# Kernel tuning notes

Hardware: AMD Instinct MI355X
Metric: run time of the kernel (lower is better)

Reference implementation:

```python
import jax, jax.numpy as jnp
import numpy as np

PATCH = 8
EPS_LN = 1e-5
EPS_NORM = 1e-12


def conv1x1(x, w):
    # x: [b,i,h,w], w: [o,i]
    return jnp.einsum('bihw,oi->bohw', x, w)


def dwconv3(x, w):
    # depthwise 3x3, SAME padding; w: [C,1,3,3]
    return jax.lax.conv_general_dilated(
        x, w, window_strides=(1, 1), padding='SAME',
        feature_group_count=x.shape[1],
        dimension_numbers=('NCHW', 'OIHW', 'NCHW'))


def l2norm(x, axis=-1):
    n = jnp.sqrt(jnp.sum(x * x, axis=axis, keepdims=True))
    return x / jnp.maximum(n, EPS_NORM)


def layernorm_ch(x, w, b):
    # WithBias LayerNorm over the channel dim of NCHW (matches to_3d/to_4d)
    mu = jnp.mean(x, axis=1, keepdims=True)
    var = jnp.mean((x - mu) ** 2, axis=1, keepdims=True)
    return (x - mu) / jnp.sqrt(var + EPS_LN) * w[None, :, None, None] + b[None, :, None, None]


def patchify(t, p):
    b, c, h, w = t.shape
    t = t.reshape(b, c, h // p, p, w // p, p)
    return t.transpose(0, 1, 2, 4, 3, 5)  # b c gh gw p p


def unpatchify(t):
    b, c, gh, gw, p1, p2 = t.shape
    return t.transpose(0, 1, 2, 4, 3, 5).reshape(b, c, gh * p1, gw * p2)


def setup_inputs() -> dict:
    key = jax.random.key(0)
    ks = jax.random.split(key, 12)
    b, c, h, w = 4, 128, 256, 256
    heads = 8
    s = 0.05
    inp = {
        'x': jax.random.normal(ks[0], (b, c, h, w), jnp.float32),
        'qkv_w': s * jax.random.normal(ks[1], (3 * c, c), jnp.float32),
        'qkv_dw': s * jax.random.normal(ks[2], (3 * c, 1, 3, 3), jnp.float32),
        'proj_w': s * jax.random.normal(ks[3], (c, c), jnp.float32),
        'q1_w': s * jax.random.normal(ks[4], (c, c), jnp.float32),
        'q2_w': s * jax.random.normal(ks[5], (c, c), jnp.float32),
        'kv_w': s * jax.random.normal(ks[6], (2 * c, c), jnp.float32),
        'kv_dw': s * jax.random.normal(ks[7], (2 * c, 1, 3, 3), jnp.float32),
        'projf_w': s * jax.random.normal(ks[8], (c, c), jnp.float32),
        'temperature': jnp.ones((1, heads, 1, 1), jnp.float32),
        'ln_w': jnp.ones((c,), jnp.float32),
        'ln_b': jnp.zeros((c,), jnp.float32),
    }
    return inp


def reference(x, qkv_w, qkv_dw, proj_w, q1_w, q2_w, kv_w, kv_dw, projf_w,
              temperature, ln_w, ln_b):
    b, c, h, w = x.shape
    heads = temperature.shape[1]
    ch = c // heads

    # ---- channel (transposed) attention ----
    qkv = dwconv3(conv1x1(x, qkv_w), qkv_dw)
    q, k, v = jnp.split(qkv, 3, axis=1)
    q = l2norm(q.reshape(b, heads, ch, h * w))
    k = l2norm(k.reshape(b, heads, ch, h * w))
    v = v.reshape(b, heads, ch, h * w)
    attn = jax.nn.softmax(jnp.einsum('bhcn,bhdn->bhcd', q, k) * temperature, axis=-1)
    out = conv1x1(jnp.einsum('bhcd,bhdn->bhcn', attn, v).reshape(b, c, h, w), proj_w)

    # ---- FFT gating branch ----
    x_fft = jnp.fft.fftn(x, axes=(-2, -1)).real
    x_fft3 = conv1x1(jax.nn.gelu(conv1x1(x_fft, q1_w), approximate=False), q2_w)
    qf = jnp.fft.ifftn(x_fft3, axes=(-2, -1)).real

    kvf = dwconv3(conv1x1(out, kv_w), kv_dw)
    kf, vf = jnp.split(kvf, 2, axis=1)

    qp = patchify(vf, PATCH)  # note: original names vf's patches q_patch_1
    kp = patchify(kf, PATCH)
    prod = jnp.fft.rfft2(qp) * jnp.fft.rfft2(kp)
    out_1 = jnp.fft.irfft2(prod, s=(PATCH, PATCH))
    out_1 = unpatchify(out_1)
    out_1 = layernorm_ch(out_1, ln_w, ln_b) * qf
    return conv1x1(out_1, projf_w) + out
```

## Files before the change

kernel.cpp:

```cpp
#include <hip/hip_runtime.h>
#include <math.h>

#define HW 65536
#define CPX 64
#define XSTR 136
#define RSTR 129

typedef short short8 __attribute__((ext_vector_type(8)));
typedef float f32x4 __attribute__((ext_vector_type(4)));

__device__ __forceinline__ float2 cmul(float2 a, float2 b){
  return make_float2(a.x*b.x - a.y*b.y, a.x*b.y + a.y*b.x);
}

__device__ __forceinline__ unsigned short f2bf(float f){
  unsigned u = __float_as_uint(f);
  u += 0x7fff + ((u >> 16) & 1);
  return (unsigned short)(u >> 16);
}
__device__ __forceinline__ float bf2f(unsigned short h){
  unsigned u = ((unsigned)h) << 16;
  return __uint_as_float(u);
}

__global__ __launch_bounds__(256,4) void conv1x1_mfma(
    const float* __restrict__ X, size_t bsX,
    const float* __restrict__ W, size_t bsW,
    float* __restrict__ Y, size_t bsY,
    const float* __restrict__ R, size_t bsR,
    int act)
{
  __shared__ __align__(16) unsigned short sbuf[2*CPX*XSTR];
  unsigned short* xh = sbuf;
  unsigned short* xl = sbuf + CPX*XSTR;
  const int t = threadIdx.x;
  const int l = t & 63;
  const int w = t >> 6;
  const int b = blockIdx.z;
  const int bx = ((blockIdx.x & 7) << 7) + (blockIdx.x >> 3);
  const size_t pxBase = (size_t)bx * CPX;
  const float* Xb = X + (size_t)b*bsX + pxBase;
  const float* Wb = W + (size_t)b*bsW;

  short8 whi[2][4], wlo[2][4];
  {
    const int row0 = (w<<5) + (l & 15);
    const int kg = (l >> 4) << 3;
    #pragma unroll
    for (int m=0;m<2;m++){
      #pragma unroll
      for (int ks=0;ks<4;ks++){
        const float* wp = Wb + (size_t)(row0 + 16*m)*128 + 32*ks + kg;
        float4 f0 = *(const float4*)wp;
        float4 f1 = *(const float4*)(wp+4);
        float fv[8] = {f0.x,f0.y,f0.z,f0.w,f1.x,f1.y,f1.z,f1.w};
        short8 h, lo;
        #pragma unroll
        for (int e=0;e<8;e++){
          unsigned short hb = f2bf(fv[e]);
          h[e]  = (short)hb;
          lo[e] = (short)f2bf(fv[e] - bf2f(hb));
        }
        whi[m][ks]=h; wlo[m][ks]=lo;
      }
    }
  }

  {
    const int px = (t & 15) << 2;
    const int s3 = (t & 7) << 3;
    #pragma unroll
    for (int i=0;i<8;i++){
      const int k = i*16 + (t >> 4);
      float4 v = *(const float4*)(Xb + (size_t)k*HW + px);
      const int kk = k ^ s3;
      float f[4] = {v.x,v.y,v.z,v.w};
      #pragma unroll
      for (int j=0;j<4;j++){
        unsigned short hb = f2bf(f[j]);
        xh[(px+j)*XSTR + kk] = hb;
        xl[(px+j)*XSTR + kk] = f2bf(f[j] - bf2f(hb));
      }
    }
  }
  __syncthreads();

  f32x4 acc[2][4];
  #pragma unroll
  for (int m=0;m<2;m++)
    #pragma unroll
    for (int n=0;n<4;n++) acc[m][n] = (f32x4){0.f,0.f,0.f,0.f};

  const int kg = (l>>4)<<3;
  #pragma unroll
  for (int ks=0;ks<4;ks++){
    const int k0 = 32*ks + kg;
    #pragma unroll
    for (int n=0;n<4;n++){
      const int px = 16*n + (l&15);
      const int off = px*XSTR + (k0 ^ (((px>>2)&7)<<3));
      short8 bh = *(short8*)&xh[off];
      short8 bl = *(short8*)&xl[off];
      #pragma unroll
      for (int m=0;m<2;m++){
        acc[m][n] = __builtin_amdgcn_mfma_f32_16x16x32_bf16(whi[m][ks], bh, acc[m][n], 0,0,0);
        acc[m][n] = __builtin_amdgcn_mfma_f32_16x16x32_bf16(wlo[m][ks], bh, acc[m][n], 0,0,0);
        acc[m][n] = __builtin_amdgcn_mfma_f32_16x16x32_bf16(whi[m][ks], bl, acc[m][n], 0,0,0);
      }
    }
  }
  __syncthreads();

  float* ost = (float*)sbuf;
  #pragma unroll
  for (int m=0;m<2;m++){
    const int ocb = (w<<5) + 16*m + ((l>>4)<<2);
    #pragma unroll
    for (int n=0;n<4;n++){
      const int px = 16*n + (l&15);
      #pragma unroll
      for (int r=0;r<4;r++){
        float v = acc[m][n][r];
        if (act==1) v = 0.5f*v*(1.f + erff(v*0.70710678118654752440f));
        ost[(ocb+r)*68 + px] = v;
      }
    }
  }
  __syncthreads();
  float* Yb = Y + (size_t)b*bsY + pxBase;
  const float* Rb = R ? (R + (size_t)b*bsR + pxBase) : 0;
  {
    const int px4 = (t & 15) << 2;
    #pragma unroll
    for (int it=0; it<8; it++){
      const int oc = it*16 + (t >> 4);
      float4 v4 = *(float4*)&ost[oc*68 + px4];
      if (Rb){
        float4 r4 = *(const float4*)(Rb + (size_t)oc*HW + px4);
        v4.x += r4.x; v4.y += r4.y; v4.z += r4.z; v4.w += r4.w;
      }
      *(float4*)(Yb + (size_t)oc*HW + px4) = v4;
    }
  }
}

__global__ __launch_bounds__(256,4) void dwconv3_row_k(
    const float* __restrict__ in, const float* __restrict__ w9,
    float* __restrict__ out, float* __restrict__ sqpart, int chOff)
{
  __shared__ float tl[34][256];
  int z = blockIdx.x;
  int cch = z & 127;
  int y0 = blockIdx.y * 32;
  size_t base = (size_t)z * HW;
  int t = threadIdx.x;
  float wv[9];
  #pragma unroll
  for (int i=0;i<9;i++) wv[i] = w9[cch*9+i];
  for (int idx = t; idx < 34*64; idx += 256){
    int r = idx >> 6, c4 = (idx & 63) << 2;
    int gy = y0 + r - 1;
    float4 v = make_float4(0.f,0.f,0.f,0.f);
    if ((unsigned)gy < 256u) v = *(const float4*)(in + base + (size_t)gy*256 + c4);
    *(float4*)&tl[r][c4] = v;
  }
  __syncthreads();
  const int ct = t;
  float ss = 0.f;
  for (int r = 0; r < 32; ++r){
    float acc = 0.f;
    #pragma unroll
    for (int dy=0; dy<3; dy++){
      float a  = (ct>0)   ? tl[r+dy][ct-1] : 0.f;
      float bm = tl[r+dy][ct];
      float c2 = (ct<255) ? tl[r+dy][ct+1] : 0.f;
      acc = fmaf(wv[dy*3+0], a, fmaf(wv[dy*3+1], bm, fmaf(wv[dy*3+2], c2, acc)));
    }
    out[base + (size_t)(y0+r)*256 + ct] = acc;
    ss += acc*acc;
  }
  if (sqpart){
    #pragma unroll
    for (int o=32;o>0;o>>=1) ss += __shfl_down(ss, o);
    __shared__ float red[4];
    if ((t&63)==0) red[t>>6] = ss;
    __syncthreads();
    if (t==0){
      float s = red[0]+red[1]+red[2]+red[3];
      int pg = ((z>>7)<<8) + chOff + cch;
      sqpart[pg*8 + blockIdx.y] = s;
    }
  }
}

__global__ __launch_bounds__(256) void qk_gram_k(
    const float* __restrict__ q, const float* __restrict__ k, float* __restrict__ Gp)
{
  __shared__ float qs[16][65], ks[16][65];
  int s = blockIdx.x, h = blockIdx.y, b = blockIdx.z;
  int t = threadIdx.x;
  int c = t >> 4, d = t & 15;
  const float* qb = q + ((size_t)b*128 + h*16)*HW + (size_t)s*1024;
  const float* kb = k + ((size_t)b*128 + h*16)*HW + (size_t)s*1024;
  float acc = 0.f;
  for (int n0=0;n0<1024;n0+=64){
    #pragma unroll
    for (int it=0;it<4;it++){
      int idx = it*256 + t;
      int row = idx >> 6, col = idx & 63;
      qs[row][col] = qb[(size_t)row*HW + n0 + col];
      ks[row][col] = kb[(size_t)row*HW + n0 + col];
    }
    __syncthreads();
    #pragma unroll
    for (int nn=0;nn<64;nn++) acc = fmaf(qs[c][nn], ks[d][nn], acc);
    __syncthreads();
  }
  Gp[(((size_t)b*8 + h)*64 + s)*256 + t] = acc;
}

__global__ __launch_bounds__(256) void attn_weff_k(
    const float* __restrict__ Gp, const float* __restrict__ sqpart,
    const float* __restrict__ temp, const float* __restrict__ proj_w,
    float* __restrict__ Weff)
{
  int b = blockIdx.x, t = threadIdx.x;
  __shared__ float G[8][16][16];
  __shared__ float A[8][16][16];
  __shared__ float rn_s[256];
  {
    const float* pp = sqpart + ((size_t)b*256 + t)*8;
    float s = 0.f;
    #pragma unroll
    for (int i=0;i<8;i++) s += pp[i];
    rn_s[t] = 1.f/fmaxf(sqrtf(s), 1e-12f);
  }
  __syncthreads();
  for (int e = t; e < 2048; e += 256){
    int h = e >> 8, cd = e & 255;
    int c = cd >> 4, d = cd & 15;
    const float* gp = Gp + (((size_t)b*8 + h)*64)*256 + cd;
    float sum = 0.f;
    for (int s2=0;s2<64;s2++) sum += gp[(size_t)s2*256];
    G[h][c][d] = sum * rn_s[h*16 + c] * rn_s[128 + h*16 + d] * temp[h];
  }
  __syncthreads();
  if (t < 128){
    int h = t >> 4, c = t & 15;
    float m = -1e30f;
    for (int d=0;d<16;d++) m = fmaxf(m, G[h][c][d]);
    float e[16], ssum = 0.f;
    for (int d=0;d<16;d++){ e[d] = expf(G[h][c][d]-m); ssum += e[d]; }
    float inv = 1.f/ssum;
    for (int d=0;d<16;d++) A[h][c][d] = e[d]*inv;
  }
  __syncthreads();
  for (int idx = t; idx < 16384; idx += 256){
    int o = idx >> 7, hd = idx & 127;
    int h = hd >> 4, d = hd & 15;
    float acc = 0.f;
    #pragma unroll
    for (int c=0;c<16;c++) acc = fmaf(proj_w[o*128 + h*16 + c], A[h][c][d], acc);
    Weff[((size_t)b*128 + o)*128 + hd] = acc;
  }
}

__global__ __launch_bounds__(256) void patch_circ_k(
    const float* __restrict__ vf, const float* __restrict__ kf, float* __restrict__ out)
{
  __shared__ float vs[32*68];
  __shared__ float ks2[32*68];
  size_t base = (size_t)blockIdx.y*HW + (size_t)blockIdx.x*2048;
  int t = threadIdx.x;
  #pragma unroll
  for (int it=0; it<2; it++){
    int idx = it*256 + t;
    int row = idx >> 6;
    int c4  = (idx & 63) << 2;
    float4 v  = *(const float4*)(vf + base + (size_t)row*256 + c4);
    float4 kv = *(const float4*)(kf + base + (size_t)row*256 + c4);
    int p = c4 >> 3, j0 = c4 & 7;
    *(float4*)&vs [p*68 + row*8 + j0] = v;
    *(float4*)&ks2[p*68 + row*8 + j0] = kv;
  }
  __syncthreads();
  int p = t & 31, pr = t >> 5;
  float acc[8];
  #pragma unroll
  for (int q=0;q<8;q++) acc[q]=0.f;
  #pragma unroll
  for (int i=0;i<8;i++){
    float4 va = *(float4*)&vs[p*68 + i*8];
    float4 vb = *(float4*)&vs[p*68 + i*8 + 4];
    int kr = (pr - i) & 7;
    float4 ka = *(float4*)&ks2[p*68 + kr*8];
    float4 kb = *(float4*)&ks2[p*68 + kr*8 + 4];
    float vv[8]={va.x,va.y,va.z,va.w,vb.x,vb.y,vb.z,vb.w};
    float kk[8]={ka.x,ka.y,ka.z,ka.w,kb.x,kb.y,kb.z,kb.w};
    #pragma unroll
    for (int q=0;q<8;q++)
      #pragma unroll
      for (int j=0;j<8;j++)
        acc[q] = fmaf(vv[j], kk[(q-j)&7], acc[q]);
  }
  float* op = out + base + (size_t)pr*256 + p*8;
  *(float4*)op     = make_float4(acc[0],acc[1],acc[2],acc[3]);
  *(float4*)(op+4) = make_float4(acc[4],acc[5],acc[6],acc[7]);
}

__global__ __launch_bounds__(64) void fft256_rows_r2c_half(
    const float* __restrict__ in, size_t inStride,
    float2* __restrict__ out, size_t outStride, float dir)
{
  __shared__ float2 buf[2][256];
  __shared__ float2 tw[128];
  int t = threadIdx.x;
  size_t row = blockIdx.x;
  const float* ip = in + (size_t)blockIdx.y*inStride + row*256;
  float2* op = out + (size_t)blockIdx.y*outStride + row*RSTR;
  for (int i = t; i < 128; i += 64){
    float ang = 6.283185307179586477f * (float)i / 256.f;
    float s, c;
    sincosf(ang, &s, &c);
    tw[i] = make_float2(c, dir*s);
  }
  for (int i=t;i<256;i+=64) buf[0][i] = make_float2(ip[i], 0.f);
  int cur = 0, m = 1;
  for (int st=0; st<8; st++){
    __syncthreads();
    #pragma unroll
    for (int p2=0;p2<2;p2++){
      int bf = t + (p2<<6);
      int k = bf & (m-1);
      int jm = bf - k;
      float2 a = buf[cur][k + jm];
      float2 c = buf[cur][k + jm + 128];
      float2 w = tw[jm];
      float2 sm = make_float2(a.x+c.x, a.y+c.y);
      float2 df = make_float2(a.x-c.x, a.y-c.y);
      buf[cur^1][k + 2*jm]     = sm;
      buf[cur^1][k + 2*jm + m] = cmul(w, df);
    }
    cur ^= 1; m <<= 1;
  }
  __syncthreads();
  for (int i=t;i<256;i+=64) if (i <= 128) op[i] = buf[cur][i];
}

__global__ __launch_bounds__(256,4) void fft256_cols_c2r_herm(
    const float2* __restrict__ in, size_t inStride,
    float* __restrict__ out, size_t outStride,
    float dir, float scale)
{
  __shared__ float2 buf[16*257];
  __shared__ float2 tw[128];
  const int t = threadIdx.x;
  const int col = t & 15, rr = t >> 4;
  const int u0 = blockIdx.x << 4;
  const int u  = u0 + col;
  const int plane = blockIdx.y;
  const bool valid = (u <= 128);
  const float2* ip = in + (size_t)blockIdx.z*inStride + (size_t)plane*(256*RSTR) + u;
  if (t < 128){
    float ang = 6.283185307179586477f * (float)t / 256.f;
    float s, c;
    sincosf(ang, &s, &c);
    tw[t] = make_float2(c, dir*s);
  }
  #pragma unroll
  for (int i=0;i<16;i++){
    int r = i*16 + rr;
    float2 v = valid ? ip[(size_t)r*RSTR] : make_float2(0.f,0.f);
    int br = __brev((unsigned)r) >> 24;
    buf[col*257 + br] = v;
  }
  __syncthreads();
  for (int s=1;s<=8;s++){
    const int half = 1 << (s-1);
    const int tsh = 8 - s;
    #pragma unroll
    for (int j=0;j<8;j++){
      int bfi = rr + (j<<4);
      int lo = bfi & (half-1);
      int p  = ((bfi >> (s-1)) << s) + lo;
      float2 uq = buf[col*257 + p];
      float2 vq = buf[col*257 + p + half];
      float2 w  = tw[lo << tsh];
      float2 wv = cmul(w, vq);
      buf[col*257 + p]        = make_float2(uq.x+wv.x, uq.y+wv.y);
      buf[col*257 + p + half] = make_float2(uq.x-wv.x, uq.y-wv.y);
    }
    __syncthreads();
  }
  float* op = out + (size_t)blockIdx.z*outStride + (size_t)plane*HW;
  if (u0 < 128){
    const int c0 = (t & 3) << 2;
    #pragma unroll
    for (int i=0;i<4;i++){
      int r = i*64 + (t >> 2);
      float4 o4 = make_float4(buf[(c0+0)*257 + r].x * scale,
                              buf[(c0+1)*257 + r].x * scale,
                              buf[(c0+2)*257 + r].x * scale,
                              buf[(c0+3)*257 + r].x * scale);
      *(float4*)(op + (size_t)r*256 + u0 + c0) = o4;
    }
    const int um = u0 + col;
    if (um >= 1 && um <= 127){
      const int mc = 256 - um;
      #pragma unroll
      for (int i=0;i<16;i++){
        int r2 = i*16 + rr;
        int src = (256 - r2) & 255;
        op[(size_t)r2*256 + mc] = buf[col*257 + src].x * scale;
      }
    }
  } else {
    int r2 = t;
    op[(size_t)r2*256 + 128] = buf[0*257 + r2].x * scale;
  }
}

__global__ __launch_bounds__(256) void ln_mul_k(
    const float* __restrict__ x, const float* __restrict__ qf,
    const float* __restrict__ lw, const float* __restrict__ lb,
    float* __restrict__ y)
{
  int b = blockIdx.y;
  size_t px0 = (size_t)blockIdx.x*64;
  int t = threadIdx.x;
  int px = t & 63, g = t >> 6;
  const float* xp = x + (size_t)b*8388608 + px0 + px;
  float vals[32];
  float s1 = 0.f, s2 = 0.f;
  #pragma unroll
  for (int i=0;i<32;i++){
    float v = xp[(size_t)(g*32+i)*HW];
    vals[i] = v; s1 += v; s2 += v*v;
  }
  __shared__ float r1[4][64], r2[4][64];
  r1[g][px] = s1; r2[g][px] = s2;
  __syncthreads();
  float S1 = r1[0][px]+r1[1][px]+r1[2][px]+r1[3][px];
  float S2 = r2[0][px]+r2[1][px]+r2[2][px]+r2[3][px];
  float mu = S1 * (1.f/128.f);
  float var = S2 * (1.f/128.f) - mu*mu;
  float rstd = rsqrtf(var + 1e-5f);
  const float* qp = qf + (size_t)b*8388608 + px0 + px;
  float* yp = y + (size_t)b*8388608 + px0 + px;
  #pragma unroll
  for (int i=0;i<32;i++){
    int c = g*32 + i;
    float v = (vals[i]-mu)*rstd*lw[c] + lb[c];
    yp[(size_t)c*HW] = v * qp[(size_t)c*HW];
  }
}

extern "C" void kernel_launch(void* const* d_in, const int* in_sizes, int n_in,
                              void* d_out, int out_size, void* d_ws, size_t ws_size,
                              hipStream_t stream)
{
  const float* x       = (const float*)d_in[0];
  const float* qkv_w   = (const float*)d_in[1];
  const float* qkv_dw  = (const float*)d_in[2];
  const float* proj_w  = (const float*)d_in[3];
  const float* q1_w    = (const float*)d_in[4];
  const float* q2_w    = (const float*)d_in[5];
  const float* kv_w    = (const float*)d_in[6];
  const float* kv_dw   = (const float*)d_in[7];
  const float* projf_w = (const float*)d_in[8];
  const float* temp    = (const float*)d_in[9];
  const float* ln_w    = (const float*)d_in[10];
  const float* ln_b    = (const float*)d_in[11];
  float* out = (float*)d_out;
  float* ws  = (float*)d_ws;

  const size_t P  = 33554432;
  const size_t CB = 8388608;
  const size_t HSTR = 32768u*RSTR;
  float* A = ws;
  float* B = ws + P;
  float* C = ws + 2*P;
  float* sqpart = ws + 3*P;
  float* Gp     = sqpart + 8192;
  float* Weff   = Gp + 524288;

  dim3 cg(1024,1,4); dim3 cb(256);
  dim3 dg(512,8);  dim3 db(256);

  conv1x1_mfma<<<cg,cb,0,stream>>>(x, CB, qkv_w + 0*16384, 0, A, CB, nullptr, 0, 0);
  dwconv3_row_k<<<dg,db,0,stream>>>(A, qkv_dw + 0*1152, out, sqpart, 0);
  conv1x1_mfma<<<cg,cb,0,stream>>>(x, CB, qkv_w + 1*16384, 0, B, CB, nullptr, 0, 0);
  dwconv3_row_k<<<dg,db,0,stream>>>(B, qkv_dw + 1*1152, A, sqpart, 128);
  qk_gram_k<<<dim3(64,8,4),256,0,stream>>>(out, A, Gp);
  attn_weff_k<<<4,256,0,stream>>>(Gp, sqpart, temp, proj_w, Weff);
  conv1x1_mfma<<<cg,cb,0,stream>>>(x, CB, qkv_w + 2*16384, 0, B, CB, nullptr, 0, 0);
  dwconv3_row_k<<<dg,db,0,stream>>>(B, qkv_dw + 2*1152, C, nullptr, 0);
  conv1x1_mfma<<<cg,cb,0,stream>>>(C, CB, Weff, 16384, B, CB, nullptr, 0, 0);
  conv1x1_mfma<<<cg,cb,0,stream>>>(B, CB, kv_w + 0*16384, 0, A, CB, nullptr, 0, 0);
  dwconv3_row_k<<<dg,db,0,stream>>>(A, kv_dw + 0*1152, out, nullptr, 0);
  conv1x1_mfma<<<cg,cb,0,stream>>>(B, CB, kv_w + 1*16384, 0, A, CB, nullptr, 0, 0);
  dwconv3_row_k<<<dg,db,0,stream>>>(A, kv_dw + 1*1152, C, nullptr, 0);
  patch_circ_k<<<dim3(32,512),256,0,stream>>>(C, out, A);
  for (int b=0;b<4;b+=2){
    fft256_rows_r2c_half<<<dim3(32768,2),64,0,stream>>>(x + (size_t)b*CB, CB, (float2*)C, HSTR, -1.f);
    fft256_cols_c2r_herm<<<dim3(9,128,2),256,0,stream>>>((const float2*)C, HSTR, out + (size_t)b*CB, CB, -1.f, 1.f);
  }
  conv1x1_mfma<<<cg,cb,0,stream>>>(out, CB, q1_w, 0, C, CB, nullptr, 0, 1);
  conv1x1_mfma<<<cg,cb,0,stream>>>(C, CB, q2_w, 0, out, CB, nullptr, 0, 0);
  for (int b=0;b<4;b+=2){
    fft256_rows_r2c_half<<<dim3(32768,2),64,0,stream>>>(out + (size_t)b*CB, CB, (float2*)C, HSTR, 1.f);
    fft256_cols_c2r_herm<<<dim3(9,128,2),256,0,stream>>>((const float2*)C, HSTR, out + (size_t)b*CB, CB, 1.f, 1.f/65536.f);
  }
  ln_mul_k<<<dim3(1024,4),256,0,stream>>>(A, out, ln_w, ln_b, C);
  conv1x1_mfma<<<cg,cb,0,stream>>>(C, CB, projf_w, 0, out, CB, B, CB, 0);
}
```

Baseline: 1.657 ms.

## Fuse multi-output 1x1 convs and pack two real rows per complex FFT

```diff
diff --git a/kernel.cpp b/kernel.cpp
--- a/kernel.cpp
+++ b/kernel.cpp
@@ -144,6 +144,123 @@
   }
 }
 
+template<int NOUT>
+__global__ __launch_bounds__(256,3) void convN_mfma(
+    const float* __restrict__ X, size_t bsX,
+    const float* __restrict__ W,
+    float* __restrict__ Y, size_t bsY, size_t ostep)
+{
+  __shared__ __align__(16) unsigned short sbuf[2*CPX*XSTR];
+  __shared__ __align__(16) float tbuf[64*68];
+  unsigned short* xh = sbuf;
+  unsigned short* xl = sbuf + CPX*XSTR;
+  const int t = threadIdx.x;
+  const int l = t & 63;
+  const int w = t >> 6;
+  const int b = blockIdx.z;
+  const int bx = ((blockIdx.x & 7) << 7) + (blockIdx.x >> 3);
+  const size_t pxBase = (size_t)bx * CPX;
+  const float* Xb = X + (size_t)b*bsX + pxBase;
+
+  {
+    const int px = (t & 15) << 2;
+    const int s3 = (t & 7) << 3;
+    #pragma unroll
+    for (int i=0;i<8;i++){
+      const int k = i*16 + (t >> 4);
+      float4 v = *(const float4*)(Xb + (size_t)k*HW + px);
+      const int kk = k ^ s3;
+      float f[4] = {v.x,v.y,v.z,v.w};
+      #pragma unroll
+      for (int j=0;j<4;j++){
+        unsigned short hb = f2bf(f[j]);
+        xh[(px+j)*XSTR + kk] = hb;
+        xl[(px+j)*XSTR + kk] = f2bf(f[j] - bf2f(hb));
+      }
+    }
+  }
+  __syncthreads();
+
+  const int kg = (l>>4)<<3;
+  const int row0 = (w<<5) + (l & 15);
+
+  #pragma unroll
+  for (int o=0; o<NOUT; ++o){
+    short8 whi[2][4], wlo[2][4];
+    {
+      const float* Wo = W + (size_t)o*16384;
+      #pragma unroll
+      for (int m=0;m<2;m++){
+        #pragma unroll
+        for (int ks=0;ks<4;ks++){
+          const float* wp = Wo + (size_t)(row0 + 16*m)*128 + 32*ks + kg;
+          float4 f0 = *(const float4*)wp;
+          float4 f1 = *(const float4*)(wp+4);
+          float fv[8] = {f0.x,f0.y,f0.z,f0.w,f1.x,f1.y,f1.z,f1.w};
+          short8 h, lo;
+          #pragma unroll
+          for (int e=0;e<8;e++){
+            unsigned short hb = f2bf(fv[e]);
+            h[e]  = (short)hb;
+            lo[e] = (short)f2bf(fv[e] - bf2f(hb));
+          }
+          whi[m][ks]=h; wlo[m][ks]=lo;
+        }
+      }
+    }
+    f32x4 acc[2][4];
+    #pragma unroll
+    for (int m=0;m<2;m++)
+      #pragma unroll
+      for (int n=0;n<4;n++) acc[m][n] = (f32x4){0.f,0.f,0.f,0.f};
+    #pragma unroll
+    for (int ks=0;ks<4;ks++){
+      const int k0 = 32*ks + kg;
+      #pragma unroll
+      for (int n=0;n<4;n++){
+        const int px = 16*n + (l&15);
+        const int off = px*XSTR + (k0 ^ (((px>>2)&7)<<3));
+        short8 bh = *(short8*)&xh[off];
+        short8 bl = *(short8*)&xl[off];
+        #pragma unroll
+        for (int m=0;m<2;m++){
+          acc[m][n] = __builtin_amdgcn_mfma_f32_16x16x32_bf16(whi[m][ks], bh, acc[m][n], 0,0,0);
+          acc[m][n] = __builtin_amdgcn_mfma_f32_16x16x32_bf16(wlo[m][ks], bh, acc[m][n], 0,0,0);
+          acc[m][n] = __builtin_amdgcn_mfma_f32_16x16x32_bf16(whi[m][ks], bl, acc[m][n], 0,0,0);
+        }
+      }
+    }
+    float* Yb = Y + (size_t)o*ostep + (size_t)b*bsY + pxBase;
+    #pragma unroll
+    for (int half=0; half<2; ++half){
+      __syncthreads();
+      if ((w >> 1) == half){
+        #pragma unroll
+        for (int m=0;m<2;m++){
+          const int ocl = ((w&1)<<5) + 16*m + ((l>>4)<<2);
+          #pragma unroll
+          for (int n=0;n<4;n++){
+            const int px = 16*n + (l&15);
+            #pragma unroll
+            for (int r=0;r<4;r++) tbuf[(ocl+r)*68 + px] = acc[m][n][r];
+          }
+        }
+      }
+      __syncthreads();
+      {
+        const int px4 = (t & 15) << 2;
+        #pragma unroll
+        for (int it=0; it<4; it++){
+          const int ocl = it*16 + (t >> 4);
+          float4 v4 = *(float4*)&tbuf[ocl*68 + px4];
+          *(float4*)(Yb + (size_t)(64*half + ocl)*HW + px4) = v4;
+        }
+      }
+    }
+    __syncthreads();
+  }
+}
+
 __global__ __launch_bounds__(256,4) void dwconv3_row_k(
     const float* __restrict__ in, const float* __restrict__ w9,
     float* __restrict__ out, float* __restrict__ sqpart, int chOff)
@@ -308,23 +425,25 @@
   *(float4*)(op+4) = make_float4(acc[4],acc[5],acc[6],acc[7]);
 }
 
-__global__ __launch_bounds__(64) void fft256_rows_r2c_half(
+__global__ __launch_bounds__(64) void fft256_rows2_r2c_half(
     const float* __restrict__ in, size_t inStride,
     float2* __restrict__ out, size_t outStride, float dir)
 {
   __shared__ float2 buf[2][256];
   __shared__ float2 tw[128];
   int t = threadIdx.x;
-  size_t row = blockIdx.x;
-  const float* ip = in + (size_t)blockIdx.y*inStride + row*256;
-  float2* op = out + (size_t)blockIdx.y*outStride + row*RSTR;
+  size_t rp = blockIdx.x;
+  const float* ipa = in + (size_t)blockIdx.y*inStride + rp*512;
+  const float* ipb = ipa + 256;
+  float2* opa = out + (size_t)blockIdx.y*outStride + rp*2*RSTR;
+  float2* opb = opa + RSTR;
   for (int i = t; i < 128; i += 64){
     float ang = 6.283185307179586477f * (float)i / 256.f;
     float s, c;
     sincosf(ang, &s, &c);
     tw[i] = make_float2(c, dir*s);
   }
-  for (int i=t;i<256;i+=64) buf[0][i] = make_float2(ip[i], 0.f);
+  for (int i=t;i<256;i+=64) buf[0][i] = make_float2(ipa[i], ipb[i]);
   int cur = 0, m = 1;
   for (int st=0; st<8; st++){
     __syncthreads();
@@ -344,7 +463,12 @@
     cur ^= 1; m <<= 1;
   }
   __syncthreads();
-  for (int i=t;i<256;i+=64) if (i <= 128) op[i] = buf[cur][i];
+  for (int u=t; u<=128; u+=64){
+    float2 z = buf[cur][u];
+    float2 mm = buf[cur][(256-u)&255];
+    opa[u] = make_float2(0.5f*(z.x+mm.x), 0.5f*(z.y-mm.y));
+    opb[u] = make_float2(0.5f*(z.y+mm.y), 0.5f*(mm.x-z.x));
+  }
 }
 
 __global__ __launch_bounds__(256,4) void fft256_cols_c2r_herm(
@@ -487,30 +611,27 @@
   dim3 cg(1024,1,4); dim3 cb(256);
   dim3 dg(512,8);  dim3 db(256);
 
-  conv1x1_mfma<<<cg,cb,0,stream>>>(x, CB, qkv_w + 0*16384, 0, A, CB, nullptr, 0, 0);
+  convN_mfma<3><<<cg,cb,0,stream>>>(x, CB, qkv_w, A, CB, P);
   dwconv3_row_k<<<dg,db,0,stream>>>(A, qkv_dw + 0*1152, out, sqpart, 0);
-  conv1x1_mfma<<<cg,cb,0,stream>>>(x, CB, qkv_w + 1*16384, 0, B, CB, nullptr, 0, 0);
   dwconv3_row_k<<<dg,db,0,stream>>>(B, qkv_dw + 1*1152, A, sqpart, 128);
   qk_gram_k<<<dim3(64,8,4),256,0,stream>>>(out, A, Gp);
   attn_weff_k<<<4,256,0,stream>>>(Gp, sqpart, temp, proj_w, Weff);
-  conv1x1_mfma<<<cg,cb,0,stream>>>(x, CB, qkv_w + 2*16384, 0, B, CB, nullptr, 0, 0);
-  dwconv3_row_k<<<dg,db,0,stream>>>(B, qkv_dw + 2*1152, C, nullptr, 0);
-  conv1x1_mfma<<<cg,cb,0,stream>>>(C, CB, Weff, 16384, B, CB, nullptr, 0, 0);
-  conv1x1_mfma<<<cg,cb,0,stream>>>(B, CB, kv_w + 0*16384, 0, A, CB, nullptr, 0, 0);
+  dwconv3_row_k<<<dg,db,0,stream>>>(C, qkv_dw + 2*1152, B, nullptr, 0);
+  conv1x1_mfma<<<cg,cb,0,stream>>>(B, CB, Weff, 16384, C, CB, nullptr, 0, 0);
+  convN_mfma<2><<<cg,cb,0,stream>>>(C, CB, kv_w, A, CB, P);
   dwconv3_row_k<<<dg,db,0,stream>>>(A, kv_dw + 0*1152, out, nullptr, 0);
-  conv1x1_mfma<<<cg,cb,0,stream>>>(B, CB, kv_w + 1*16384, 0, A, CB, nullptr, 0, 0);
-  dwconv3_row_k<<<dg,db,0,stream>>>(A, kv_dw + 1*1152, C, nullptr, 0);
-  patch_circ_k<<<dim3(32,512),256,0,stream>>>(C, out, A);
+  dwconv3_row_k<<<dg,db,0,stream>>>(B, kv_dw + 1*1152, A, nullptr, 0);
+  patch_circ_k<<<dim3(32,512),256,0,stream>>>(A, out, B);
   for (int b=0;b<4;b+=2){
-    fft256_rows_r2c_half<<<dim3(32768,2),64,0,stream>>>(x + (size_t)b*CB, CB, (float2*)C, HSTR, -1.f);
-    fft256_cols_c2r_herm<<<dim3(9,128,2),256,0,stream>>>((const float2*)C, HSTR, out + (size_t)b*CB, CB, -1.f, 1.f);
-  }
-  conv1x1_mfma<<<cg,cb,0,stream>>>(out, CB, q1_w, 0, C, CB, nullptr, 0, 1);
-  conv1x1_mfma<<<cg,cb,0,stream>>>(C, CB, q2_w, 0, out, CB, nullptr, 0, 0);
+    fft256_rows2_r2c_half<<<dim3(16384,2),64,0,stream>>>(x + (size_t)b*CB, CB, (float2*)A, HSTR, -1.f);
+    fft256_cols_c2r_herm<<<dim3(9,128,2),256,0,stream>>>((const float2*)A, HSTR, out + (size_t)b*CB, CB, -1.f, 1.f);
+  }
+  conv1x1_mfma<<<cg,cb,0,stream>>>(out, CB, q1_w, 0, A, CB, nullptr, 0, 1);
+  conv1x1_mfma<<<cg,cb,0,stream>>>(A, CB, q2_w, 0, out, CB, nullptr, 0, 0);
   for (int b=0;b<4;b+=2){
-    fft256_rows_r2c_half<<<dim3(32768,2),64,0,stream>>>(out + (size_t)b*CB, CB, (float2*)C, HSTR, 1.f);
-    fft256_cols_c2r_herm<<<dim3(9,128,2),256,0,stream>>>((const float2*)C, HSTR, out + (size_t)b*CB, CB, 1.f, 1.f/65536.f);
-  }
-  ln_mul_k<<<dim3(1024,4),256,0,stream>>>(A, out, ln_w, ln_b, C);
-  conv1x1_mfma<<<cg,cb,0,stream>>>(C, CB, projf_w, 0, out, CB, B, CB, 0);
-}
+    fft256_rows2_r2c_half<<<dim3(16384,2),64,0,stream>>>(out + (size_t)b*CB, CB, (float2*)A, HSTR, 1.f);
+    fft256_cols_c2r_herm<<<dim3(9,128,2),256,0,stream>>>((const float2*)A, HSTR, out + (size_t)b*CB, CB, 1.f, 1.f/65536.f);
+  }
+  ln_mul_k<<<dim3(1024,4),256,0,stream>>>(B, out, ln_w, ln_b, A);
+  conv1x1_mfma<<<cg,cb,0,stream>>>(A, CB, projf_w, 0, out, CB, C, CB, 0);
+}
```

Result: faster. 1.538 ms (-7.2%).
